# Performance work log

Hardware: AMD Instinct MI355X
Metric: run time of the kernel (lower is better)

## Reference

```python
import jax, jax.numpy as jnp
import numpy as np

B, A, R, I, V = 256, 196, 1024, 1024, 10000  # batch, att_size, rnn_size, input_size, output_size


def _lin_init(key, out_dim, in_dim):
    kw, kb = jax.random.split(key)
    s = 1.0 / np.sqrt(in_dim)
    w = jax.random.uniform(kw, (out_dim, in_dim), jnp.float32, -s, s)
    b = jax.random.uniform(kb, (out_dim,), jnp.float32, -s, s)
    return w, b


def setup_inputs() -> dict:
    key = jax.random.key(0)
    ks = jax.random.split(key, 11)
    x = jax.random.normal(ks[0], (B, I), jnp.float32)
    att = jax.random.normal(ks[1], (B, A, R), jnp.float32)
    prev_c = jax.random.normal(ks[2], (B, R), jnp.float32)
    prev_h = jax.random.normal(ks[3], (B, R), jnp.float32)
    a2a_w, a2a_b = _lin_init(ks[4], A, R)
    h2a_w, h2a_b = _lin_init(ks[5], A, R)
    d2d_w, d2d_b = _lin_init(ks[6], 1, A)
    i2h_w, i2h_b = _lin_init(ks[7], 4 * R, I)
    h2h_w, h2h_b = _lin_init(ks[8], 4 * R, R)
    r2a_w, r2a_b = _lin_init(ks[9], 4 * R, R)
    proj_w, proj_b = _lin_init(ks[10], V, R)
    return dict(x=x, att=att, prev_c=prev_c, prev_h=prev_h,
                a2a_w=a2a_w, a2a_b=a2a_b, h2a_w=h2a_w, h2a_b=h2a_b,
                d2d_w=d2d_w, d2d_b=d2d_b, i2h_w=i2h_w, i2h_b=i2h_b,
                h2h_w=h2h_w, h2h_b=h2h_b, r2a_w=r2a_w, r2a_b=r2a_b,
                proj_w=proj_w, proj_b=proj_b)


def reference(x, att, prev_c, prev_h, a2a_w, a2a_b, h2a_w, h2a_b,
              d2d_w, d2d_b, i2h_w, i2h_b, h2h_w, h2h_b,
              r2a_w, r2a_b, proj_w, proj_b):
    # Bahdanau-style attention: att [B, A, R]
    att_v = jnp.einsum('bir,ar->bia', att, a2a_w) + a2a_b      # [B, A, A]
    att_h = prev_h @ h2a_w.T + h2a_b                            # [B, A]
    dot = jnp.tanh(att_h[:, :, None] + att_v)                   # [B, A, A]
    score = jnp.einsum('bia,a->bi', dot, d2d_w[0]) + d2d_b[0]   # [B, A]
    weight = jax.nn.softmax(score, axis=1)                      # [B, A]
    att_res = jnp.einsum('bir,bi->br', att, weight)             # [B, R]
    # LSTM cell gating
    sums = (x @ i2h_w.T + i2h_b) + (prev_h @ h2h_w.T + h2h_b) + (att_res @ r2a_w.T + r2a_b)
    in_gate = jax.nn.sigmoid(sums[:, 0:R])
    forget_gate = jax.nn.sigmoid(sums[:, R:2 * R])
    out_gate = jax.nn.sigmoid(sums[:, 2 * R:3 * R])
    in_transform = jnp.tanh(sums[:, 3 * R:4 * R])
    next_c = forget_gate * prev_c + in_gate * in_transform
    next_h = out_gate * jnp.tanh(next_c)
    logsoft = jax.nn.log_softmax(next_h @ proj_w.T + proj_b, axis=1)
    return (next_c, next_h, logsoft)
```

## Files before the change

kernel.cpp:

```cpp
#include <hip/hip_runtime.h>
#include <math.h>

#define B_ 256
#define A_ 196
#define R_ 1024
#define V_ 10000
#define G4 4096
#define M_ (B_ * A_)

typedef __bf16 bf16x8 __attribute__((ext_vector_type(8)));
typedef float f32x4 __attribute__((ext_vector_type(4)));

#define OFF_ATTH   0
#define OFF_SCORE  50176
#define OFF_WEIGHT 100352
#define OFF_ATTRES 150528
#define OFF_P0     412672
#define OFF_P1     1461248
#define OFF_NHBF   2509824
#define OFF_LOGITS 2640896
#define OFF_PACKA  5200896
#define OFF_PACKH  5307392

__device__ __forceinline__ float tanh_fast(float x) {
    float e = __expf(2.f * x);
    return 1.f - 2.f / (e + 1.f);
}
__device__ __forceinline__ float sigmoid_fast(float x) {
    return 1.f / (1.f + __expf(-x));
}

__device__ __forceinline__ bf16x8 cvt8(float4 f0, float4 f1) {
    bf16x8 v;
    v[0] = (__bf16)f0.x; v[1] = (__bf16)f0.y; v[2] = (__bf16)f0.z; v[3] = (__bf16)f0.w;
    v[4] = (__bf16)f1.x; v[5] = (__bf16)f1.y; v[6] = (__bf16)f1.z; v[7] = (__bf16)f1.w;
    return v;
}

__global__ void pack_kernel(const float* __restrict__ a2a_w,
                            const float* __restrict__ h2a_w,
                            __bf16* __restrict__ packA,
                            __bf16* __restrict__ packH) {
    int row = blockIdx.x;
    int c = threadIdx.x * 4;
    if (row < 208) {
        float4 f = (row < A_) ? *(const float4*)(a2a_w + (size_t)row * R_ + c)
                              : make_float4(0.f, 0.f, 0.f, 0.f);
        __bf16* p = packA + (size_t)row * R_ + c;
        p[0] = (__bf16)f.x; p[1] = (__bf16)f.y; p[2] = (__bf16)f.z; p[3] = (__bf16)f.w;
    } else {
        int r2 = row - 208;
        float4 f = (r2 < A_) ? *(const float4*)(h2a_w + (size_t)r2 * R_ + c)
                             : make_float4(0.f, 0.f, 0.f, 0.f);
        __bf16* p = packH + (size_t)r2 * R_ + c;
        p[0] = (__bf16)f.x; p[1] = (__bf16)f.y; p[2] = (__bf16)f.z; p[3] = (__bf16)f.w;
    }
}

__global__ __launch_bounds__(256)
void att_h_gemm(const float* __restrict__ prev_h,
                const __bf16* __restrict__ packH,
                const float* __restrict__ h2a_b,
                float* __restrict__ att_h) {
    __shared__ alignas(16) __bf16 As[64][40];
    __shared__ alignas(16) __bf16 Bs[64][40];
    int tid = threadIdx.x;
    int m0 = blockIdx.x * 64, n0 = blockIdx.y * 64;
    int lane = tid & 63, w = tid >> 6, ln = lane & 15, quad = lane >> 4;
    int arow = tid >> 2, akq = (tid & 3) * 8;

    f32x4 acc[4];
#pragma unroll
    for (int t = 0; t < 4; ++t) acc[t] = {0.f, 0.f, 0.f, 0.f};

    const float* Asrc = prev_h + (size_t)(m0 + arow) * R_ + akq;
    const __bf16* Bsrc = packH + (size_t)(n0 + arow) * R_ + akq;

    float4 pa0 = *(const float4*)Asrc;
    float4 pa1 = *(const float4*)(Asrc + 4);
    bf16x8 pb = *(const bf16x8*)Bsrc;

    for (int k0 = 0; k0 < R_; k0 += 32) {
        __syncthreads();
        *(bf16x8*)&As[arow][akq] = cvt8(pa0, pa1);
        *(bf16x8*)&Bs[arow][akq] = pb;
        __syncthreads();
        if (k0 + 32 < R_) {
            pa0 = *(const float4*)(Asrc + k0 + 32);
            pa1 = *(const float4*)(Asrc + k0 + 36);
            pb = *(const bf16x8*)(Bsrc + k0 + 32);
        }
        bf16x8 a = *(bf16x8*)&As[w * 16 + ln][quad * 8];
#pragma unroll
        for (int t = 0; t < 4; ++t) {
            bf16x8 b = *(bf16x8*)&Bs[t * 16 + ln][quad * 8];
            acc[t] = __builtin_amdgcn_mfma_f32_16x16x32_bf16(a, b, acc[t], 0, 0, 0);
        }
    }
#pragma unroll
    for (int t = 0; t < 4; ++t) {
#pragma unroll
        for (int r = 0; r < 4; ++r) {
            int m = m0 + w * 16 + quad * 4 + r;
            int n = n0 + t * 16 + ln;
            if (n < A_) att_h[m * A_ + n] = acc[t][r] + h2a_b[n];
        }
    }
}

__global__ __launch_bounds__(256)
void score_gemm_mfma(const float* __restrict__ att,
                     const __bf16* __restrict__ packA,
                     const float* __restrict__ a2a_b,
                     const float* __restrict__ d2d_w,
                     const float* __restrict__ att_h,
                     float* __restrict__ score) {
    __shared__ alignas(16) char Bs[2][20480];
    int tid = threadIdx.x;
    int m0 = blockIdx.x * 64;
    int lane = tid & 63, w = tid >> 6, ln = lane & 15, quad = lane >> 4;

    const char* packAb = (const char*)packA;
    unsigned goff[5], loff[5];
#pragma unroll
    for (int j = 0; j < 5; ++j) {
        unsigned o = (unsigned)((w * 5 + j) * 1024 + lane * 16);
        unsigned row = o / 80u;
        unsigned ci = (o % 80u) / 16u;
        loff[j] = o;
        goff[j] = (row < 208u && ci < 4u) ? (row * 2048u + ci * 16u) : 0u;
    }

    const float* Ap = att + (size_t)(m0 + w * 16 + ln) * R_ + quad * 8;

    f32x4 acc[13];
#pragma unroll
    for (int t = 0; t < 13; ++t) acc[t] = {0.f, 0.f, 0.f, 0.f};

#pragma unroll
    for (int j = 0; j < 5; ++j)
        __builtin_amdgcn_global_load_lds(
            (const __attribute__((address_space(1))) void*)(packAb + goff[j]),
            (__attribute__((address_space(3))) void*)(&Bs[0][0] + loff[j]), 16, 0, 0);
    asm volatile("" ::: "memory");
    float4 c0 = *(const float4*)Ap;
    float4 c1 = *(const float4*)(Ap + 4);
    asm volatile("" ::: "memory");
#pragma unroll
    for (int j = 0; j < 5; ++j)
        __builtin_amdgcn_global_load_lds(
            (const __attribute__((address_space(1))) void*)(packAb + goff[j] + 64),
            (__attribute__((address_space(3))) void*)(&Bs[1][0] + loff[j]), 16, 0, 0);
    asm volatile("" ::: "memory");

    for (int p = 0; p < 32; ++p) {
        int cur = p & 1;
        const char* bufc = &Bs[cur][0];
        float4 n0 = c0, n1 = c1;
        if (p + 1 < 32) {
            n0 = *(const float4*)(Ap + (p + 1) * 32);
            n1 = *(const float4*)(Ap + (p + 1) * 32 + 4);
        }
        if (p + 1 < 32)
            asm volatile("s_waitcnt vmcnt(7)" ::: "memory");
        else
            asm volatile("s_waitcnt vmcnt(0)" ::: "memory");
        bf16x8 a = cvt8(c0, c1);
        asm volatile("s_barrier" ::: "memory");
        const char* bp = bufc + ln * 80 + quad * 16;
#pragma unroll
        for (int t = 0; t < 13; ++t) {
            bf16x8 b = *(const bf16x8*)(bp + t * 1280);
            acc[t] = __builtin_amdgcn_mfma_f32_16x16x32_bf16(a, b, acc[t], 0, 0, 0);
        }
        c0 = n0; c1 = n1;
        asm volatile("s_barrier" ::: "memory");
        if (p + 2 < 32) {
            unsigned kb = (unsigned)(p + 2) * 64u;
#pragma unroll
            for (int j = 0; j < 5; ++j)
                __builtin_amdgcn_global_load_lds(
                    (const __attribute__((address_space(1))) void*)(packAb + goff[j] + kb),
                    (__attribute__((address_space(3))) void*)(bufc + loff[j]), 16, 0, 0);
        }
        asm volatile("" ::: "memory");
    }

    float wv[13], bb[13];
#pragma unroll
    for (int t = 0; t < 13; ++t) {
        int n = t * 16 + ln;
        wv[t] = (n < A_) ? d2d_w[n] : 0.f;
        bb[t] = (n < A_) ? a2a_b[n] : 0.f;
    }
#pragma unroll
    for (int r = 0; r < 4; ++r) {
        int m = m0 + w * 16 + quad * 4 + r;
        float ah = att_h[m];
        float p = 0.f;
#pragma unroll
        for (int t = 0; t < 13; ++t)
            p += tanh_fast(acc[t][r] + bb[t] + ah) * wv[t];
        p += __shfl_xor(p, 1);
        p += __shfl_xor(p, 2);
        p += __shfl_xor(p, 4);
        p += __shfl_xor(p, 8);
        if (ln == 0) score[m] = p;
    }
}

__global__ void softmax_kernel(const float* __restrict__ score,
                               const float* __restrict__ d2d_b,
                               float* __restrict__ weight) {
    int b = blockIdx.x;
    int i = threadIdx.x;
    __shared__ float red[256];
    float sval = 0.f;
    float s = -1e30f;
    if (i < A_) {
        sval = score[b * A_ + i] + d2d_b[0];
        s = sval;
    }
    red[i] = s; __syncthreads();
    for (int off = 128; off > 0; off >>= 1) {
        if (i < off) red[i] = fmaxf(red[i], red[i + off]);
        __syncthreads();
    }
    float mx = red[0]; __syncthreads();
    float e = (i < A_) ? __expf(sval - mx) : 0.f;
    red[i] = e; __syncthreads();
    for (int off = 128; off > 0; off >>= 1) {
        if (i < off) red[i] += red[i + off];
        __syncthreads();
    }
    float inv = 1.f / red[0];
    if (i < A_) weight[b * A_ + i] = e * inv;
}

__global__ __launch_bounds__(256)
void att_res_kernel(const float* __restrict__ att,
                    const float* __restrict__ weight,
                    float* __restrict__ att_res) {
    int b = blockIdx.x;
    int r = blockIdx.y * 512 + threadIdx.x * 2;
    __shared__ float wsm[A_];
    if (threadIdx.x < A_) wsm[threadIdx.x] = weight[b * A_ + threadIdx.x];
    __syncthreads();
    const float* ap = att + (size_t)b * A_ * R_ + r;
    float acx = 0.f, acy = 0.f;
    for (int i = 0; i < A_; i += 4) {
        float2 v0 = *(const float2*)(ap + (size_t)(i + 0) * R_);
        float2 v1 = *(const float2*)(ap + (size_t)(i + 1) * R_);
        float2 v2 = *(const float2*)(ap + (size_t)(i + 2) * R_);
        float2 v3 = *(const float2*)(ap + (size_t)(i + 3) * R_);
        float w0 = wsm[i], w1 = wsm[i + 1], w2 = wsm[i + 2], w3 = wsm[i + 3];
        acx += v0.x * w0 + v1.x * w1 + v2.x * w2 + v3.x * w3;
        acy += v0.y * w0 + v1.y * w1 + v2.y * w2 + v3.y * w3;
    }
    *(float2*)(att_res + (size_t)b * R_ + r) = make_float2(acx, acy);
}

__global__ __launch_bounds__(256)
void sums_gemm_mfma(const float* __restrict__ x,
                    const float* __restrict__ prev_h,
                    const float* __restrict__ att_res,
                    const float* __restrict__ i2h_w,
                    const float* __restrict__ h2h_w,
                    const float* __restrict__ r2a_w,
                    float* __restrict__ P0,
                    float* __restrict__ P1) {
    __shared__ alignas(16) __bf16 As[64][40];
    __shared__ alignas(16) __bf16 Bs[64][40];
    int tid = threadIdx.x;
    int m0 = blockIdx.x * 64, n0 = blockIdx.y * 64;
    int ks = blockIdx.z;
    int kbeg = ks * 512, kend = kbeg + 512;
    int lane = tid & 63, w = tid >> 6, ln = lane & 15, quad = lane >> 4;
    int arow = tid >> 2, akq = (tid & 3) * 8;

    f32x4 acc[4];
#pragma unroll
    for (int t = 0; t < 4; ++t) acc[t] = {0.f, 0.f, 0.f, 0.f};

    const float* Al[3] = {x, prev_h, att_res};
    const float* Bl[3] = {i2h_w, h2h_w, r2a_w};
    for (int p = 0; p < 3; ++p) {
        const float* Asrc = Al[p] + (size_t)(m0 + arow) * R_ + akq;
        const float* Bsrc = Bl[p] + (size_t)(n0 + arow) * R_ + akq;
        float4 pa0 = *(const float4*)(Asrc + kbeg);
        float4 pa1 = *(const float4*)(Asrc + kbeg + 4);
        float4 pb0 = *(const float4*)(Bsrc + kbeg);
        float4 pb1 = *(const float4*)(Bsrc + kbeg + 4);
        for (int k0 = kbeg; k0 < kend; k0 += 32) {
            __syncthreads();
            *(bf16x8*)&As[arow][akq] = cvt8(pa0, pa1);
            *(bf16x8*)&Bs[arow][akq] = cvt8(pb0, pb1);
            __syncthreads();
            if (k0 + 32 < kend) {
                pa0 = *(const float4*)(Asrc + k0 + 32);
                pa1 = *(const float4*)(Asrc + k0 + 36);
                pb0 = *(const float4*)(Bsrc + k0 + 32);
                pb1 = *(const float4*)(Bsrc + k0 + 36);
            }
            bf16x8 a = *(bf16x8*)&As[w * 16 + ln][quad * 8];
#pragma unroll
            for (int t = 0; t < 4; ++t) {
                bf16x8 b = *(bf16x8*)&Bs[t * 16 + ln][quad * 8];
                acc[t] = __builtin_amdgcn_mfma_f32_16x16x32_bf16(a, b, acc[t], 0, 0, 0);
            }
        }
    }
    float* P = ks ? P1 : P0;
#pragma unroll
    for (int t = 0; t < 4; ++t) {
#pragma unroll
        for (int r = 0; r < 4; ++r) {
            int m = m0 + w * 16 + quad * 4 + r;
            int n = n0 + t * 16 + ln;
            P[(size_t)m * G4 + n] = acc[t][r];
        }
    }
}

__global__ void gates_kernel(const float* __restrict__ P0,
                             const float* __restrict__ P1,
                             const float* __restrict__ i2h_b,
                             const float* __restrict__ h2h_b,
                             const float* __restrict__ r2a_b,
                             const float* __restrict__ prev_c,
                             float* __restrict__ out_c,
                             float* __restrict__ out_h,
                             __bf16* __restrict__ nh_bf) {
    int idx = blockIdx.x * 256 + threadIdx.x;
    int b = idx >> 10, r = idx & 1023;
    size_t off = (size_t)b * G4;
    float s0 = P0[off + r] + P1[off + r] + i2h_b[r] + h2h_b[r] + r2a_b[r];
    float s1 = P0[off + R_ + r] + P1[off + R_ + r] + i2h_b[R_ + r] + h2h_b[R_ + r] + r2a_b[R_ + r];
    float s2 = P0[off + 2 * R_ + r] + P1[off + 2 * R_ + r] + i2h_b[2 * R_ + r] + h2h_b[2 * R_ + r] + r2a_b[2 * R_ + r];
    float s3 = P0[off + 3 * R_ + r] + P1[off + 3 * R_ + r] + i2h_b[3 * R_ + r] + h2h_b[3 * R_ + r] + r2a_b[3 * R_ + r];
    float ig = sigmoid_fast(s0);
    float fg = sigmoid_fast(s1);
    float og = sigmoid_fast(s2);
    float it = tanh_fast(s3);
    float nc = fg * prev_c[idx] + ig * it;
    float nh = og * tanh_fast(nc);
    out_c[idx] = nc;
    out_h[idx] = nh;
    nh_bf[idx] = (__bf16)nh;
}

__global__ __launch_bounds__(256)
void proj_gemm_mfma(const __bf16* __restrict__ nh_bf,
                    const float* __restrict__ proj_w,
                    const float* __restrict__ proj_b,
                    float* __restrict__ logits) {
    __shared__ alignas(16) __bf16 As[64][40];
    __shared__ alignas(16) __bf16 Bs[64][40];
    int tid = threadIdx.x;
    int m0 = blockIdx.x * 64, n0 = blockIdx.y * 64;
    int lane = tid & 63, w = tid >> 6, ln = lane & 15, quad = lane >> 4;
    int arow = tid >> 2, akq = (tid & 3) * 8;

    f32x4 acc[4];
#pragma unroll
    for (int t = 0; t < 4; ++t) acc[t] = {0.f, 0.f, 0.f, 0.f};

    int nr = n0 + arow;
    int nrc = nr < V_ ? nr : V_ - 1;
    const __bf16* Asrc = nh_bf + (size_t)(m0 + arow) * R_ + akq;
    const float* Bsrc = proj_w + (size_t)nrc * R_ + akq;

    bf16x8 pa = *(const bf16x8*)Asrc;
    float4 pb0 = *(const float4*)Bsrc;
    float4 pb1 = *(const float4*)(Bsrc + 4);

    for (int k0 = 0; k0 < R_; k0 += 32) {
        __syncthreads();
        *(bf16x8*)&As[arow][akq] = pa;
        *(bf16x8*)&Bs[arow][akq] = cvt8(pb0, pb1);
        __syncthreads();
        if (k0 + 32 < R_) {
            pa = *(const bf16x8*)(Asrc + k0 + 32);
            pb0 = *(const float4*)(Bsrc + k0 + 32);
            pb1 = *(const float4*)(Bsrc + k0 + 36);
        }
        bf16x8 a = *(bf16x8*)&As[w * 16 + ln][quad * 8];
#pragma unroll
        for (int t = 0; t < 4; ++t) {
            bf16x8 b = *(bf16x8*)&Bs[t * 16 + ln][quad * 8];
            acc[t] = __builtin_amdgcn_mfma_f32_16x16x32_bf16(a, b, acc[t], 0, 0, 0);
        }
    }
#pragma unroll
    for (int t = 0; t < 4; ++t) {
#pragma unroll
        for (int r = 0; r < 4; ++r) {
            int m = m0 + w * 16 + quad * 4 + r;
            int n = n0 + t * 16 + ln;
            if (n < V_) logits[(size_t)m * V_ + n] = acc[t][r] + proj_b[n];
        }
    }
}

__global__ void logsoftmax_kernel(const float* __restrict__ logits,
                                  float* __restrict__ out) {
    int b = blockIdx.x, t = threadIdx.x;
    __shared__ float red[256];
    const float* lp = logits + (size_t)b * V_;
    float mx = -1e30f;
    for (int v = t; v < V_; v += 256) mx = fmaxf(mx, lp[v]);
    red[t] = mx; __syncthreads();
    for (int off = 128; off > 0; off >>= 1) {
        if (t < off) red[t] = fmaxf(red[t], red[t + off]);
        __syncthreads();
    }
    mx = red[0]; __syncthreads();
    float s = 0.f;
    for (int v = t; v < V_; v += 256) s += __expf(lp[v] - mx);
    red[t] = s; __syncthreads();
    for (int off = 128; off > 0; off >>= 1) {
        if (t < off) red[t] += red[t + off];
        __syncthreads();
    }
    float lse = mx + __logf(red[0]);
    float* op = out + (size_t)b * V_;
    for (int v = t; v < V_; v += 256) op[v] = lp[v] - lse;
}

extern "C" void kernel_launch(void* const* d_in, const int* in_sizes, int n_in,
                              void* d_out, int out_size, void* d_ws, size_t ws_size,
                              hipStream_t stream) {
    const float* x      = (const float*)d_in[0];
    const float* att    = (const float*)d_in[1];
    const float* prev_c = (const float*)d_in[2];
    const float* prev_h = (const float*)d_in[3];
    const float* a2a_w  = (const float*)d_in[4];
    const float* a2a_b  = (const float*)d_in[5];
    const float* h2a_w  = (const float*)d_in[6];
    const float* h2a_b  = (const float*)d_in[7];
    const float* d2d_w  = (const float*)d_in[8];
    const float* d2d_b  = (const float*)d_in[9];
    const float* i2h_w  = (const float*)d_in[10];
    const float* i2h_b  = (const float*)d_in[11];
    const float* h2h_w  = (const float*)d_in[12];
    const float* h2h_b  = (const float*)d_in[13];
    const float* r2a_w  = (const float*)d_in[14];
    const float* r2a_b  = (const float*)d_in[15];
    const float* proj_w = (const float*)d_in[16];
    const float* proj_b = (const float*)d_in[17];

    float* ws      = (float*)d_ws;
    float* att_h   = ws + OFF_ATTH;
    float* score   = ws + OFF_SCORE;
    float* weight  = ws + OFF_WEIGHT;
    float* att_res = ws + OFF_ATTRES;
    float* P0      = ws + OFF_P0;
    float* P1      = ws + OFF_P1;
    __bf16* nh_bf  = (__bf16*)(ws + OFF_NHBF);
    float* logits  = ws + OFF_LOGITS;
    __bf16* packA  = (__bf16*)(ws + OFF_PACKA);
    __bf16* packH  = (__bf16*)(ws + OFF_PACKH);
    float* out     = (float*)d_out;

    pack_kernel<<<464, 256, 0, stream>>>(a2a_w, h2a_w, packA, packH);
    att_h_gemm<<<dim3(B_ / 64, 4), 256, 0, stream>>>(prev_h, packH, h2a_b, att_h);
    score_gemm_mfma<<<M_ / 64, 256, 0, stream>>>(att, packA, a2a_b, d2d_w, att_h, score);
    softmax_kernel<<<B_, 256, 0, stream>>>(score, d2d_b, weight);
    att_res_kernel<<<dim3(B_, 2), 256, 0, stream>>>(att, weight, att_res);
    sums_gemm_mfma<<<dim3(B_ / 64, G4 / 64, 2), 256, 0, stream>>>(
        x, prev_h, att_res, i2h_w, h2h_w, r2a_w, P0, P1);
    gates_kernel<<<(B_ * R_) / 256, 256, 0, stream>>>(
        P0, P1, i2h_b, h2h_b, r2a_b, prev_c, out, out + B_ * R_, nh_bf);
    proj_gemm_mfma<<<dim3(B_ / 64, (V_ + 63) / 64), 256, 0, stream>>>(
        nh_bf, proj_w, proj_b, logits);
    logsoftmax_kernel<<<B_, 256, 0, stream>>>(logits, out + 2 * B_ * R_);
}
```

Measured before the change: 570.9 us.

## Deepen att A-operand prefetch to four stages with unrolled phase loop

The attention score GEMM loop now keeps four register slots of att rows in flight instead of one, unrolling the 32-step K loop by four so each phase issues the load for step p+4. The waitcnt is loosened to vmcnt(9) to match the deeper queue, and the B-tile LDS loads are issued every step with a clamped index instead of a conditional. The goal is to hide global load latency for the streaming att read at the cost of more registers and some redundant tail loads.

```diff
diff --git a/kernel.cpp b/kernel.cpp
--- a/kernel.cpp
+++ b/kernel.cpp
@@ -143,8 +143,8 @@
             (const __attribute__((address_space(1))) void*)(packAb + goff[j]),
             (__attribute__((address_space(3))) void*)(&Bs[0][0] + loff[j]), 16, 0, 0);
     asm volatile("" ::: "memory");
-    float4 c0 = *(const float4*)Ap;
-    float4 c1 = *(const float4*)(Ap + 4);
+    float4 sa0_0 = *(const float4*)Ap;
+    float4 sa0_1 = *(const float4*)(Ap + 4);
     asm volatile("" ::: "memory");
 #pragma unroll
     for (int j = 0; j < 5; ++j)
@@ -152,39 +152,51 @@
             (const __attribute__((address_space(1))) void*)(packAb + goff[j] + 64),
             (__attribute__((address_space(3))) void*)(&Bs[1][0] + loff[j]), 16, 0, 0);
     asm volatile("" ::: "memory");
-
-    for (int p = 0; p < 32; ++p) {
-        int cur = p & 1;
-        const char* bufc = &Bs[cur][0];
-        float4 n0 = c0, n1 = c1;
-        if (p + 1 < 32) {
-            n0 = *(const float4*)(Ap + (p + 1) * 32);
-            n1 = *(const float4*)(Ap + (p + 1) * 32 + 4);
-        }
-        if (p + 1 < 32)
-            asm volatile("s_waitcnt vmcnt(7)" ::: "memory");
-        else
-            asm volatile("s_waitcnt vmcnt(0)" ::: "memory");
-        bf16x8 a = cvt8(c0, c1);
-        asm volatile("s_barrier" ::: "memory");
-        const char* bp = bufc + ln * 80 + quad * 16;
-#pragma unroll
-        for (int t = 0; t < 13; ++t) {
-            bf16x8 b = *(const bf16x8*)(bp + t * 1280);
-            acc[t] = __builtin_amdgcn_mfma_f32_16x16x32_bf16(a, b, acc[t], 0, 0, 0);
-        }
-        c0 = n0; c1 = n1;
-        asm volatile("s_barrier" ::: "memory");
-        if (p + 2 < 32) {
-            unsigned kb = (unsigned)(p + 2) * 64u;
-#pragma unroll
-            for (int j = 0; j < 5; ++j)
-                __builtin_amdgcn_global_load_lds(
-                    (const __attribute__((address_space(1))) void*)(packAb + goff[j] + kb),
-                    (__attribute__((address_space(3))) void*)(bufc + loff[j]), 16, 0, 0);
-        }
-        asm volatile("" ::: "memory");
-    }
+    float4 sa1_0 = *(const float4*)(Ap + 32);
+    float4 sa1_1 = *(const float4*)(Ap + 36);
+    float4 sa2_0 = *(const float4*)(Ap + 64);
+    float4 sa2_1 = *(const float4*)(Ap + 68);
+    float4 sa3_0 = *(const float4*)(Ap + 96);
+    float4 sa3_1 = *(const float4*)(Ap + 100);
+    asm volatile("" ::: "memory");
+
+#define PHASE(J, S0, S1)                                                      \
+    {                                                                         \
+        int p = p4 + J;                                                       \
+        bf16x8 a = cvt8(S0, S1);              \
+        int pn = p + 4; if (pn > 31) pn = 31;                                 \
+        S0 = *(const float4*)(Ap + pn * 32);                                  \
+        S1 = *(const float4*)(Ap + pn * 32 + 4);                              \
+        asm volatile("" ::: "memory");                                        \
+        asm volatile("s_waitcnt vmcnt(9)" ::: "memory");                      \
+        asm volatile("s_barrier" ::: "memory");                               \
+        const char* bp = &Bs[J & 1][0] + ln * 80 + quad * 16;                 \
+        _Pragma("unroll")                                                     \
+        for (int t = 0; t < 13; ++t) {                                        \
+            bf16x8 b = *(const bf16x8*)(bp + t * 1280);                       \
+            acc[t] = __builtin_amdgcn_mfma_f32_16x16x32_bf16(a, b, acc[t], 0, 0, 0); \
+        }                                                                     \
+        asm volatile("s_barrier" ::: "memory");                               \
+        {                                                                     \
+            int kp = p + 2; if (kp > 31) kp = 31;                             \
+            unsigned kb = (unsigned)kp * 64u;                                 \
+            char* dst = &Bs[J & 1][0];                                        \
+            _Pragma("unroll")                                                 \
+            for (int jj = 0; jj < 5; ++jj)                                    \
+                __builtin_amdgcn_global_load_lds(                             \
+                    (const __attribute__((address_space(1))) void*)(packAb + goff[jj] + kb), \
+                    (__attribute__((address_space(3))) void*)(dst + loff[jj]), 16, 0, 0);    \
+        }                                                                     \
+        asm volatile("" ::: "memory");                                        \
+    }
+
+    for (int p4 = 0; p4 < 32; p4 += 4) {
+        PHASE(0, sa0_0, sa0_1)
+        PHASE(1, sa1_0, sa1_1)
+        PHASE(2, sa2_0, sa2_1)
+        PHASE(3, sa3_0, sa3_1)
+    }
+#undef PHASE
 
     float wv[13], bb[13];
 #pragma unroll
```

Measured after the change: 555.3 us. 1.03x faster.

## Fuse attention score GEMM, softmax and weighted sum into one per-batch kernel

Applied to the files above, without the earlier changes.

Replaces the score GEMM, softmax and att_res kernels with a single kernel that uses one 512-thread block per batch item. Each wave handles 32 attention rows, reads the packed a2a weights straight from global memory instead of staging them through LDS, keeps the scores in shared memory, and then does the softmax and the weighted sum over att in the same block. This removes two launches and the global round-trips for score and weight, and the second pass over att may hit in cache. In exchange, grid parallelism drops from 784 blocks to 256, the weight tile is no longer shared across waves through LDS, and each wave holds 26 accumulator registers.

```diff
diff --git a/kernel.cpp b/kernel.cpp
--- a/kernel.cpp
+++ b/kernel.cpp
@@ -108,156 +108,124 @@
     }
 }
 
-__global__ __launch_bounds__(256)
-void score_gemm_mfma(const float* __restrict__ att,
-                     const __bf16* __restrict__ packA,
-                     const float* __restrict__ a2a_b,
-                     const float* __restrict__ d2d_w,
-                     const float* __restrict__ att_h,
-                     float* __restrict__ score) {
-    __shared__ alignas(16) char Bs[2][20480];
-    int tid = threadIdx.x;
-    int m0 = blockIdx.x * 64;
-    int lane = tid & 63, w = tid >> 6, ln = lane & 15, quad = lane >> 4;
-
-    const char* packAb = (const char*)packA;
-    unsigned goff[5], loff[5];
-#pragma unroll
-    for (int j = 0; j < 5; ++j) {
-        unsigned o = (unsigned)((w * 5 + j) * 1024 + lane * 16);
-        unsigned row = o / 80u;
-        unsigned ci = (o % 80u) / 16u;
-        loff[j] = o;
-        goff[j] = (row < 208u && ci < 4u) ? (row * 2048u + ci * 16u) : 0u;
-    }
-
-    const float* Ap = att + (size_t)(m0 + w * 16 + ln) * R_ + quad * 8;
-
-    f32x4 acc[13];
-#pragma unroll
-    for (int t = 0; t < 13; ++t) acc[t] = {0.f, 0.f, 0.f, 0.f};
-
-#pragma unroll
-    for (int j = 0; j < 5; ++j)
-        __builtin_amdgcn_global_load_lds(
-            (const __attribute__((address_space(1))) void*)(packAb + goff[j]),
-            (__attribute__((address_space(3))) void*)(&Bs[0][0] + loff[j]), 16, 0, 0);
-    asm volatile("" ::: "memory");
-    float4 c0 = *(const float4*)Ap;
-    float4 c1 = *(const float4*)(Ap + 4);
-    asm volatile("" ::: "memory");
-#pragma unroll
-    for (int j = 0; j < 5; ++j)
-        __builtin_amdgcn_global_load_lds(
-            (const __attribute__((address_space(1))) void*)(packAb + goff[j] + 64),
-            (__attribute__((address_space(3))) void*)(&Bs[1][0] + loff[j]), 16, 0, 0);
-    asm volatile("" ::: "memory");
+__global__ __launch_bounds__(512, 1)
+void att_fused(const float* __restrict__ att,
+               const __bf16* __restrict__ packA,
+               const float* __restrict__ a2a_b,
+               const float* __restrict__ d2d_w,
+               const float* __restrict__ d2d_b,
+               const float* __restrict__ att_h,
+               float* __restrict__ att_res) {
+    __shared__ float sm[256];
+    __shared__ float red[512];
+    const int b = blockIdx.x;
+    const int tid = threadIdx.x;
+    const int w = tid >> 6, lane = tid & 63, ln = lane & 15, quad = lane >> 4;
+
+    int r0 = w * 32 + ln;        int r0c = r0 < A_ ? r0 : A_ - 1;
+    int r1 = w * 32 + 16 + ln;   int r1c = r1 < A_ ? r1 : A_ - 1;
+    const float* Ap0 = att + (size_t)(b * A_ + r0c) * R_ + quad * 8;
+    const float* Ap1 = att + (size_t)(b * A_ + r1c) * R_ + quad * 8;
+    const __bf16* Bb = packA + (size_t)ln * R_ + quad * 8;
+
+    f32x4 acc0[13], acc1[13];
+#pragma unroll
+    for (int t = 0; t < 13; ++t) {
+        acc0[t] = {0.f, 0.f, 0.f, 0.f};
+        acc1[t] = {0.f, 0.f, 0.f, 0.f};
+    }
+
+    float4 a00 = *(const float4*)Ap0, a01 = *(const float4*)(Ap0 + 4);
+    float4 a10 = *(const float4*)Ap1, a11 = *(const float4*)(Ap1 + 4);
 
     for (int p = 0; p < 32; ++p) {
-        int cur = p & 1;
-        const char* bufc = &Bs[cur][0];
-        float4 n0 = c0, n1 = c1;
-        if (p + 1 < 32) {
-            n0 = *(const float4*)(Ap + (p + 1) * 32);
-            n1 = *(const float4*)(Ap + (p + 1) * 32 + 4);
-        }
-        if (p + 1 < 32)
-            asm volatile("s_waitcnt vmcnt(7)" ::: "memory");
-        else
-            asm volatile("s_waitcnt vmcnt(0)" ::: "memory");
-        bf16x8 a = cvt8(c0, c1);
-        asm volatile("s_barrier" ::: "memory");
-        const char* bp = bufc + ln * 80 + quad * 16;
-#pragma unroll
-        for (int t = 0; t < 13; ++t) {
-            bf16x8 b = *(const bf16x8*)(bp + t * 1280);
-            acc[t] = __builtin_amdgcn_mfma_f32_16x16x32_bf16(a, b, acc[t], 0, 0, 0);
-        }
-        c0 = n0; c1 = n1;
-        asm volatile("s_barrier" ::: "memory");
-        if (p + 2 < 32) {
-            unsigned kb = (unsigned)(p + 2) * 64u;
-#pragma unroll
-            for (int j = 0; j < 5; ++j)
-                __builtin_amdgcn_global_load_lds(
-                    (const __attribute__((address_space(1))) void*)(packAb + goff[j] + kb),
-                    (__attribute__((address_space(3))) void*)(bufc + loff[j]), 16, 0, 0);
-        }
-        asm volatile("" ::: "memory");
-    }
-
-    float wv[13], bb[13];
+        bf16x8 bt0[7];
+#pragma unroll
+        for (int t = 0; t < 7; ++t)
+            bt0[t] = *(const bf16x8*)(Bb + (size_t)t * 16 * R_ + p * 32);
+        int pn = p + 1 < 32 ? p + 1 : 31;
+        float4 n00 = *(const float4*)(Ap0 + pn * 32);
+        float4 n01 = *(const float4*)(Ap0 + pn * 32 + 4);
+        float4 n10 = *(const float4*)(Ap1 + pn * 32);
+        float4 n11 = *(const float4*)(Ap1 + pn * 32 + 4);
+        bf16x8 bt1[6];
+#pragma unroll
+        for (int t = 0; t < 6; ++t)
+            bt1[t] = *(const bf16x8*)(Bb + (size_t)(t + 7) * 16 * R_ + p * 32);
+        bf16x8 af0 = cvt8(a00, a01);
+        bf16x8 af1 = cvt8(a10, a11);
+#pragma unroll
+        for (int t = 0; t < 7; ++t) {
+            acc0[t] = __builtin_amdgcn_mfma_f32_16x16x32_bf16(af0, bt0[t], acc0[t], 0, 0, 0);
+            acc1[t] = __builtin_amdgcn_mfma_f32_16x16x32_bf16(af1, bt0[t], acc1[t], 0, 0, 0);
+        }
+#pragma unroll
+        for (int t = 0; t < 6; ++t) {
+            acc0[t + 7] = __builtin_amdgcn_mfma_f32_16x16x32_bf16(af0, bt1[t], acc0[t + 7], 0, 0, 0);
+            acc1[t + 7] = __builtin_amdgcn_mfma_f32_16x16x32_bf16(af1, bt1[t], acc1[t + 7], 0, 0, 0);
+        }
+        a00 = n00; a01 = n01; a10 = n10; a11 = n11;
+    }
+
+    float wv[13], bb2[13];
 #pragma unroll
     for (int t = 0; t < 13; ++t) {
         int n = t * 16 + ln;
         wv[t] = (n < A_) ? d2d_w[n] : 0.f;
-        bb[t] = (n < A_) ? a2a_b[n] : 0.f;
-    }
-#pragma unroll
-    for (int r = 0; r < 4; ++r) {
-        int m = m0 + w * 16 + quad * 4 + r;
-        float ah = att_h[m];
-        float p = 0.f;
-#pragma unroll
-        for (int t = 0; t < 13; ++t)
-            p += tanh_fast(acc[t][r] + bb[t] + ah) * wv[t];
-        p += __shfl_xor(p, 1);
-        p += __shfl_xor(p, 2);
-        p += __shfl_xor(p, 4);
-        p += __shfl_xor(p, 8);
-        if (ln == 0) score[m] = p;
-    }
-}
-
-__global__ void softmax_kernel(const float* __restrict__ score,
-                               const float* __restrict__ d2d_b,
-                               float* __restrict__ weight) {
-    int b = blockIdx.x;
-    int i = threadIdx.x;
-    __shared__ float red[256];
-    float sval = 0.f;
-    float s = -1e30f;
-    if (i < A_) {
-        sval = score[b * A_ + i] + d2d_b[0];
-        s = sval;
-    }
-    red[i] = s; __syncthreads();
-    for (int off = 128; off > 0; off >>= 1) {
-        if (i < off) red[i] = fmaxf(red[i], red[i + off]);
+        bb2[t] = (n < A_) ? a2a_b[n] : 0.f;
+    }
+#pragma unroll
+    for (int mf = 0; mf < 2; ++mf) {
+#pragma unroll
+        for (int r = 0; r < 4; ++r) {
+            int slot = w * 32 + mf * 16 + quad * 4 + r;
+            float ah = (slot < A_) ? att_h[b * A_ + slot] : 0.f;
+            float pv = 0.f;
+#pragma unroll
+            for (int t = 0; t < 13; ++t) {
+                float v = (mf == 0) ? acc0[t][r] : acc1[t][r];
+                pv += tanh_fast(v + bb2[t] + ah) * wv[t];
+            }
+            pv += __shfl_xor(pv, 1);
+            pv += __shfl_xor(pv, 2);
+            pv += __shfl_xor(pv, 4);
+            pv += __shfl_xor(pv, 8);
+            if (ln == 0 && slot < A_) sm[slot] = pv;
+        }
+    }
+    __syncthreads();
+
+    float sval = 0.f, s = -1e30f;
+    if (tid < A_) { sval = sm[tid] + d2d_b[0]; s = sval; }
+    red[tid] = s; __syncthreads();
+    for (int off = 256; off > 0; off >>= 1) {
+        if (tid < off) red[tid] = fmaxf(red[tid], red[tid + off]);
         __syncthreads();
     }
     float mx = red[0]; __syncthreads();
-    float e = (i < A_) ? __expf(sval - mx) : 0.f;
-    red[i] = e; __syncthreads();
-    for (int off = 128; off > 0; off >>= 1) {
-        if (i < off) red[i] += red[i + off];
+    float e = (tid < A_) ? __expf(sval - mx) : 0.f;
+    red[tid] = e; __syncthreads();
+    for (int off = 256; off > 0; off >>= 1) {
+        if (tid < off) red[tid] += red[tid + off];
         __syncthreads();
     }
     float inv = 1.f / red[0];
-    if (i < A_) weight[b * A_ + i] = e * inv;
-}
-
-__global__ __launch_bounds__(256)
-void att_res_kernel(const float* __restrict__ att,
-                    const float* __restrict__ weight,
-                    float* __restrict__ att_res) {
-    int b = blockIdx.x;
-    int r = blockIdx.y * 512 + threadIdx.x * 2;
-    __shared__ float wsm[A_];
-    if (threadIdx.x < A_) wsm[threadIdx.x] = weight[b * A_ + threadIdx.x];
+    if (tid < A_) sm[tid] = e * inv;
     __syncthreads();
-    const float* ap = att + (size_t)b * A_ * R_ + r;
+
+    int rr = tid * 2;
+    const float* ap = att + (size_t)b * A_ * R_ + rr;
     float acx = 0.f, acy = 0.f;
     for (int i = 0; i < A_; i += 4) {
         float2 v0 = *(const float2*)(ap + (size_t)(i + 0) * R_);
         float2 v1 = *(const float2*)(ap + (size_t)(i + 1) * R_);
         float2 v2 = *(const float2*)(ap + (size_t)(i + 2) * R_);
         float2 v3 = *(const float2*)(ap + (size_t)(i + 3) * R_);
-        float w0 = wsm[i], w1 = wsm[i + 1], w2 = wsm[i + 2], w3 = wsm[i + 3];
+        float w0 = sm[i], w1 = sm[i + 1], w2 = sm[i + 2], w3 = sm[i + 3];
         acx += v0.x * w0 + v1.x * w1 + v2.x * w2 + v3.x * w3;
         acy += v0.y * w0 + v1.y * w1 + v2.y * w2 + v3.y * w3;
     }
-    *(float2*)(att_res + (size_t)b * R_ + r) = make_float2(acx, acy);
+    *(float2*)(att_res + (size_t)b * R_ + rr) = make_float2(acx, acy);
 }
 
 __global__ __launch_bounds__(256)
@@ -451,8 +419,6 @@
 
     float* ws      = (float*)d_ws;
     float* att_h   = ws + OFF_ATTH;
-    float* score   = ws + OFF_SCORE;
-    float* weight  = ws + OFF_WEIGHT;
     float* att_res = ws + OFF_ATTRES;
     float* P0      = ws + OFF_P0;
     float* P1      = ws + OFF_P1;
@@ -464,9 +430,7 @@
 
     pack_kernel<<<464, 256, 0, stream>>>(a2a_w, h2a_w, packA, packH);
     att_h_gemm<<<dim3(B_ / 64, 4), 256, 0, stream>>>(prev_h, packH, h2a_b, att_h);
-    score_gemm_mfma<<<M_ / 64, 256, 0, stream>>>(att, packA, a2a_b, d2d_w, att_h, score);
-    softmax_kernel<<<B_, 256, 0, stream>>>(score, d2d_b, weight);
-    att_res_kernel<<<dim3(B_, 2), 256, 0, stream>>>(att, weight, att_res);
+    att_fused<<<B_, 512, 0, stream>>>(att, packA, a2a_b, d2d_w, d2d_b, att_h, att_res);
     sums_gemm_mfma<<<dim3(B_ / 64, G4 / 64, 2), 256, 0, stream>>>(
         x, prev_h, att_res, i2h_w, h2h_w, r2a_w, P0, P1);
     gates_kernel<<<(B_ * R_) / 256, 256, 0, stream>>>(
```

Result: no change. 575.8 us (+0.9%).
